# Kernel optimization log

Measured on AMD Instinct MI355X. Metric: run time of the kernel, lower is better.

The kernel has to match this reference:

```python
import jax, jax.numpy as jnp
import numpy as np

N_NODES = 100000
N_EDGES = 1600000
N_GRAPHS = 64
IN_DIM = 128
HIDDEN = 64
OUT_DIM = 6


def gcn_conv(x, W, b, src, dst, n_nodes):
    """PyG GCNConv: D^{-1/2} (A + I) D^{-1/2} X W + b (self-loops added)."""
    xw = x @ W  # [N, H]
    # degree including self-loop (computed over destination nodes)
    deg = jax.ops.segment_sum(jnp.ones((src.shape[0],), xw.dtype), dst,
                              num_segments=n_nodes) + 1.0
    dinv = jax.lax.rsqrt(deg)  # deg >= 1, always safe
    # per-edge normalized messages, scatter-add into destinations
    coef = (dinv[src] * dinv[dst])[:, None]  # [E, 1]
    agg = jax.ops.segment_sum(xw[src] * coef, dst, num_segments=n_nodes)
    # self-loop contribution: dinv[i]^2 * xw[i]
    agg = agg + xw * (dinv * dinv)[:, None]
    return agg + b


def setup_inputs() -> dict:
    key = jax.random.key(0)
    ks = jax.random.split(key, 9)
    x = jax.random.normal(ks[0], (N_NODES, IN_DIM), dtype=jnp.float32)
    edge_index = jax.random.randint(ks[1], (2, N_EDGES), 0, N_NODES, dtype=jnp.int64)
    batch = jnp.sort(jax.random.randint(ks[2], (N_NODES,), 0, N_GRAPHS, dtype=jnp.int64))
    # Glorot-ish params
    W1 = jax.random.normal(ks[3], (IN_DIM, HIDDEN), dtype=jnp.float32) / np.sqrt(IN_DIM)
    b1 = jnp.zeros((HIDDEN,), jnp.float32)
    W2 = jax.random.normal(ks[4], (HIDDEN, HIDDEN), dtype=jnp.float32) / np.sqrt(HIDDEN)
    b2 = jnp.zeros((HIDDEN,), jnp.float32)
    Wl = jax.random.normal(ks[5], (HIDDEN, OUT_DIM), dtype=jnp.float32) / np.sqrt(HIDDEN)
    bl = jnp.zeros((OUT_DIM,), jnp.float32)
    return {"x": x, "edge_index": edge_index, "batch": batch,
            "W1": W1, "b1": b1, "W2": W2, "b2": b2, "Wl": Wl, "bl": bl}


def reference(x, edge_index, batch, W1, b1, W2, b2, Wl, bl):
    src, dst = edge_index[0], edge_index[1]
    h = jax.nn.relu(gcn_conv(x, W1, b1, src, dst, N_NODES))
    # dropout is identity in eval mode
    h = gcn_conv(h, W2, b2, src, dst, N_NODES)
    # global mean pool over graph ids
    sums = jax.ops.segment_sum(h, batch, num_segments=N_GRAPHS)  # [G, H]
    cnts = jax.ops.segment_sum(jnp.ones((h.shape[0],), h.dtype), batch,
                               num_segments=N_GRAPHS)
    pooled = sums / jnp.maximum(cnts, 1.0)[:, None]
    return pooled @ Wl + bl  # [G, OUT_DIM]
```

## Files before the change

### kernel.cpp

```cpp
#include <hip/hip_runtime.h>

#define NCOL 64
#define BSH 8
#define NBMAX 512
#define EPB 2048
#define P2CAP 6144


__device__ __forceinline__ unsigned int bf16pair(float a, float b) {
  unsigned int ua = __float_as_uint(a), ub = __float_as_uint(b);
  ua = (ua + 0x7FFFu + ((ua >> 16) & 1u)) >> 16;
  ub = (ub + 0x7FFFu + ((ub >> 16) & 1u)) >> 16;
  return (ub << 16) | ua;
}
__device__ __forceinline__ float bf_lo(unsigned int v) { return __uint_as_float(v << 16); }
__device__ __forceinline__ float bf_hi(unsigned int v) { return __uint_as_float(v & 0xFFFF0000u); }


__global__ __launch_bounds__(256) void bin_p1(const int* __restrict__ src,
                                              const int* __restrict__ dst,
                                              unsigned int* __restrict__ ent,
                                              int* __restrict__ blockOff,
                                              int ne, int nb) {
  __shared__ int hist[NBMAX];
  __shared__ int base[NBMAX];
  __shared__ int part[256];
  __shared__ unsigned int stage[EPB];
  int tid = threadIdx.x;
  int e0 = blockIdx.x * EPB;
  int cnt = min(EPB, ne - e0);

  for (int i = tid; i < NBMAX; i += 256) hist[i] = 0;
  __syncthreads();
  for (int i = tid; i < cnt; i += 256) {
    int d = dst[e0 + i];
    atomicAdd(&hist[d >> BSH], 1);
  }
  __syncthreads();

  int a0 = hist[2 * tid], a1 = hist[2 * tid + 1];
  int s = a0 + a1;
  part[tid] = s;
  __syncthreads();
  for (int d = 1; d < 256; d <<= 1) {
    int v = (tid >= d) ? part[tid - d] : 0;
    __syncthreads();
    part[tid] += v;
    __syncthreads();
  }
  int off = part[tid] - s;
  base[2 * tid] = off;
  base[2 * tid + 1] = off + a0;
  __syncthreads();

  for (int b = tid; b < nb; b += 256) blockOff[(size_t)blockIdx.x * nb + b] = base[b];
  for (int i = tid; i < NBMAX; i += 256) hist[i] = base[i];
  __syncthreads();

  for (int i = tid; i < cnt; i += 256) {
    int d = dst[e0 + i];
    int sv = src[e0 + i];
    unsigned int e = ((unsigned int)(d & ((1 << BSH) - 1)) << 17) | (unsigned int)sv;
    int p = atomicAdd(&hist[d >> BSH], 1);
    stage[p] = e;
  }
  __syncthreads();
  for (int i = tid; i < cnt; i += 256) ent[e0 + i] = stage[i];
}


__global__ __launch_bounds__(256) void deg_bin(const unsigned int* __restrict__ ent,
                                               const int* __restrict__ blockOff,
                                               int* __restrict__ degi,
                                               int n, int ne, int nb, int nblk) {
  __shared__ int cnt[256];
  int b = blockIdx.x;
  int tid = threadIdx.x;
  cnt[tid] = 0;
  __syncthreads();
  for (int blk = tid; blk < nblk; blk += 256) {
    int e0 = blk * EPB;
    int bcnt = min(EPB, ne - e0);
    int st = blockOff[(size_t)blk * nb + b];
    int en = (b + 1 < nb) ? blockOff[(size_t)blk * nb + b + 1] : bcnt;
    for (int i = st; i < en; ++i) {
      unsigned int e = ent[e0 + i];
      atomicAdd(&cnt[e >> 17], 1);
    }
  }
  __syncthreads();
  int node = (b << BSH) + tid;
  if (node < n) degi[node] = cnt[tid];
}

__global__ void dinv_kernel(const int* __restrict__ degi, float* __restrict__ dinv, int n) {
  int i = blockIdx.x * blockDim.x + threadIdx.x;
  if (i < n) dinv[i] = rsqrtf((float)degi[i] + 1.0f);
}


__global__ void bounds_kernel(const int* __restrict__ batch, int* __restrict__ startg,
                              int* __restrict__ endg, int n) {
  int i = blockIdx.x * blockDim.x + threadIdx.x;
  if (i >= n) return;
  int b = batch[i];
  if (i == 0) {
    startg[b] = 0;
  } else {
    int bp = batch[i - 1];
    if (b != bp) { startg[b] = i; endg[bp] = i; }
  }
  if (i == n - 1) endg[b] = n;
}


#define SCAN_C 8

__global__ void scan_part(const int* __restrict__ degi, int* __restrict__ tsum,
                          int n, int nthreads) {
  int t = blockIdx.x * blockDim.x + threadIdx.x;
  if (t >= nthreads) return;
  int lo = t * SCAN_C, hi = min(lo + SCAN_C, n);
  int s = 0;
  for (int i = lo; i < hi; ++i) s += degi[i];
  tsum[t] = s;
}

__global__ void scan_mid(int* __restrict__ tsum, int* __restrict__ toff, int nthreads) {
  __shared__ int part[1024];
  int t = threadIdx.x;
  int chunk = (nthreads + 1023) >> 10;
  int lo = t * chunk, hi = min(lo + chunk, nthreads);
  int s = 0;
  for (int i = lo; i < hi; ++i) s += tsum[i];
  part[t] = s;
  __syncthreads();
  for (int d = 1; d < 1024; d <<= 1) {
    int v = (t >= d) ? part[t - d] : 0;
    __syncthreads();
    part[t] += v;
    __syncthreads();
  }
  int off = part[t] - s;
  for (int i = lo; i < hi; ++i) { toff[i] = off; off += tsum[i]; }
}

__global__ void scan_fill(const int* __restrict__ degi, const int* __restrict__ toff,
                          int* __restrict__ rowptr, int n, int nthreads) {
  int t = blockIdx.x * blockDim.x + threadIdx.x;
  if (t >= nthreads) return;
  int lo = t * SCAN_C, hi = min(lo + SCAN_C, n);
  int off = toff[t];
  for (int i = lo; i < hi; ++i) {
    rowptr[i] = off;
    off += degi[i];
  }
  if (hi == n) rowptr[n] = off;
}


__global__ __launch_bounds__(256) void bin_p2(const unsigned int* __restrict__ ent,
                                              const int* __restrict__ blockOff,
                                              const int* __restrict__ rowptr,
                                              int* __restrict__ csr_src,
                                              int n, int ne, int nb, int nblk) {
  __shared__ int cur[256];
  __shared__ int outS[P2CAP];
  int b = blockIdx.x;
  int tid = threadIdx.x;
  int node0 = b << BSH;
  int node1 = min(node0 + 256, n);
  int bucketBase = rowptr[node0];
  int bucketCnt = rowptr[node1] - bucketBase;
  int node = node0 + tid;
  cur[tid] = (node < node1) ? (rowptr[node] - bucketBase) : 0;
  __syncthreads();
  for (int blk = tid; blk < nblk; blk += 256) {
    int e0 = blk * EPB;
    int bcnt = min(EPB, ne - e0);
    int st = blockOff[(size_t)blk * nb + b];
    int en = (b + 1 < nb) ? blockOff[(size_t)blk * nb + b + 1] : bcnt;
    for (int i = st; i < en; ++i) {
      unsigned int e = ent[e0 + i];
      int dL = e >> 17;
      int sv = (int)(e & 0x1FFFFu);
      int p = atomicAdd(&cur[dL], 1);
      if (p < P2CAP) outS[p] = sv;
      else csr_src[bucketBase + p] = sv;
    }
  }
  __syncthreads();
  int lim = min(bucketCnt, P2CAP);
  for (int i = tid; i < lim; i += 256) csr_src[bucketBase + i] = outS[i];
}


template<int K>
__global__ __launch_bounds__(256, 4) void gemm_tiled(
    const float* __restrict__ X, const float* __restrict__ W,
    const float* __restrict__ dinv, unsigned int* __restrict__ Ybf, int n) {
  __shared__ float XS[64][65];
  __shared__ float WS[64][68];
  int tid = threadIdx.x;
  int rows0 = blockIdx.x * 64;
  int tr = tid & 15;
  int tc = tid >> 4;

  float acc[4][4];
#pragma unroll
  for (int i = 0; i < 4; ++i)
#pragma unroll
    for (int j = 0; j < 4; ++j) acc[i][j] = 0.f;

  int r0 = tid >> 4;
  int c4 = (tid & 15) * 4;

  for (int ks = 0; ks < K; ks += 64) {
    if (ks) __syncthreads();
#pragma unroll
    for (int it = 0; it < 4; ++it) {
      int r = r0 + it * 16;
      int gr2 = min(rows0 + r, n - 1);
      float4 v = *reinterpret_cast<const float4*>(X + (size_t)gr2 * K + ks + c4);
      XS[r][c4 + 0] = v.x; XS[r][c4 + 1] = v.y;
      XS[r][c4 + 2] = v.z; XS[r][c4 + 3] = v.w;
      float4 wv = *reinterpret_cast<const float4*>(W + (size_t)(ks + r) * NCOL + c4);
      WS[r][c4 + 0] = wv.x; WS[r][c4 + 1] = wv.y;
      WS[r][c4 + 2] = wv.z; WS[r][c4 + 3] = wv.w;
    }
    __syncthreads();

#pragma unroll 4
    for (int k = 0; k < 64; k += 2) {
      float a0 = XS[4 * tr + 0][k], a1 = XS[4 * tr + 1][k];
      float a2 = XS[4 * tr + 2][k], a3 = XS[4 * tr + 3][k];
      float b0 = XS[4 * tr + 0][k + 1], b1 = XS[4 * tr + 1][k + 1];
      float b2 = XS[4 * tr + 2][k + 1], b3 = XS[4 * tr + 3][k + 1];
      float4 w0 = *reinterpret_cast<const float4*>(&WS[k][4 * tc]);
      float4 w1 = *reinterpret_cast<const float4*>(&WS[k + 1][4 * tc]);
      acc[0][0] = fmaf(a0, w0.x, acc[0][0]); acc[0][1] = fmaf(a0, w0.y, acc[0][1]);
      acc[0][2] = fmaf(a0, w0.z, acc[0][2]); acc[0][3] = fmaf(a0, w0.w, acc[0][3]);
      acc[1][0] = fmaf(a1, w0.x, acc[1][0]); acc[1][1] = fmaf(a1, w0.y, acc[1][1]);
      acc[1][2] = fmaf(a1, w0.z, acc[1][2]); acc[1][3] = fmaf(a1, w0.w, acc[1][3]);
      acc[2][0] = fmaf(a2, w0.x, acc[2][0]); acc[2][1] = fmaf(a2, w0.y, acc[2][1]);
      acc[2][2] = fmaf(a2, w0.z, acc[2][2]); acc[2][3] = fmaf(a2, w0.w, acc[2][3]);
      acc[3][0] = fmaf(a3, w0.x, acc[3][0]); acc[3][1] = fmaf(a3, w0.y, acc[3][1]);
      acc[3][2] = fmaf(a3, w0.z, acc[3][2]); acc[3][3] = fmaf(a3, w0.w, acc[3][3]);
      acc[0][0] = fmaf(b0, w1.x, acc[0][0]); acc[0][1] = fmaf(b0, w1.y, acc[0][1]);
      acc[0][2] = fmaf(b0, w1.z, acc[0][2]); acc[0][3] = fmaf(b0, w1.w, acc[0][3]);
      acc[1][0] = fmaf(b1, w1.x, acc[1][0]); acc[1][1] = fmaf(b1, w1.y, acc[1][1]);
      acc[1][2] = fmaf(b1, w1.z, acc[1][2]); acc[1][3] = fmaf(b1, w1.w, acc[1][3]);
      acc[2][0] = fmaf(b2, w1.x, acc[2][0]); acc[2][1] = fmaf(b2, w1.y, acc[2][1]);
      acc[2][2] = fmaf(b2, w1.z, acc[2][2]); acc[2][3] = fmaf(b2, w1.w, acc[2][3]);
      acc[3][0] = fmaf(b3, w1.x, acc[3][0]); acc[3][1] = fmaf(b3, w1.y, acc[3][1]);
      acc[3][2] = fmaf(b3, w1.z, acc[3][2]); acc[3][3] = fmaf(b3, w1.w, acc[3][3]);
    }
  }

#pragma unroll
  for (int i = 0; i < 4; ++i) {
    int gr = rows0 + 4 * tr + i;
    if (gr < n) {
      float d = dinv[gr];
      uint2 o;
      o.x = bf16pair(acc[i][0] * d, acc[i][1] * d);
      o.y = bf16pair(acc[i][2] * d, acc[i][3] * d);
      *reinterpret_cast<uint2*>(Ybf + (size_t)gr * (NCOL / 2) + 2 * tc) = o;
    }
  }
}


template<bool RELU>
__global__ __launch_bounds__(256) void aggregate(
    const int* __restrict__ rowptr, const int* __restrict__ csr_src,
    const uint4* __restrict__ Ybf4, const float* __restrict__ dinv,
    const float* __restrict__ bias, float* __restrict__ H, int n) {
  int nd = (blockIdx.x * blockDim.x + threadIdx.x) >> 3;
  if (nd >= n) return;
  int l = threadIdx.x & 7;
  int lo = rowptr[nd], hi = rowptr[nd + 1];

  uint4 vs = Ybf4[(size_t)nd * 8 + l];
  float a0 = bf_lo(vs.x), a1 = bf_hi(vs.x);
  float a2 = bf_lo(vs.y), a3 = bf_hi(vs.y);
  float a4 = bf_lo(vs.z), a5 = bf_hi(vs.z);
  float a6 = bf_lo(vs.w), a7 = bf_hi(vs.w);

  int p = lo;
  for (; p + 3 < hi; p += 4) {
    int s0 = csr_src[p];
    int s1 = csr_src[p + 1];
    int s2 = csr_src[p + 2];
    int s3 = csr_src[p + 3];
    uint4 v0 = Ybf4[(size_t)s0 * 8 + l];
    uint4 v1 = Ybf4[(size_t)s1 * 8 + l];
    uint4 v2 = Ybf4[(size_t)s2 * 8 + l];
    uint4 v3 = Ybf4[(size_t)s3 * 8 + l];
    a0 += bf_lo(v0.x); a1 += bf_hi(v0.x);
    a2 += bf_lo(v0.y); a3 += bf_hi(v0.y);
    a4 += bf_lo(v0.z); a5 += bf_hi(v0.z);
    a6 += bf_lo(v0.w); a7 += bf_hi(v0.w);
    a0 += bf_lo(v1.x); a1 += bf_hi(v1.x);
    a2 += bf_lo(v1.y); a3 += bf_hi(v1.y);
    a4 += bf_lo(v1.z); a5 += bf_hi(v1.z);
    a6 += bf_lo(v1.w); a7 += bf_hi(v1.w);
    a0 += bf_lo(v2.x); a1 += bf_hi(v2.x);
    a2 += bf_lo(v2.y); a3 += bf_hi(v2.y);
    a4 += bf_lo(v2.z); a5 += bf_hi(v2.z);
    a6 += bf_lo(v2.w); a7 += bf_hi(v2.w);
    a0 += bf_lo(v3.x); a1 += bf_hi(v3.x);
    a2 += bf_lo(v3.y); a3 += bf_hi(v3.y);
    a4 += bf_lo(v3.z); a5 += bf_hi(v3.z);
    a6 += bf_lo(v3.w); a7 += bf_hi(v3.w);
  }
  for (; p < hi; ++p) {
    int s = csr_src[p];
    uint4 v = Ybf4[(size_t)s * 8 + l];
    a0 += bf_lo(v.x); a1 += bf_hi(v.x);
    a2 += bf_lo(v.y); a3 += bf_hi(v.y);
    a4 += bf_lo(v.z); a5 += bf_hi(v.z);
    a6 += bf_lo(v.w); a7 += bf_hi(v.w);
  }

  float d = dinv[nd];
  float4 b0 = *reinterpret_cast<const float4*>(bias + l * 8);
  float4 b1 = *reinterpret_cast<const float4*>(bias + l * 8 + 4);
  float4 o0, o1;
  o0.x = fmaf(d, a0, b0.x); o0.y = fmaf(d, a1, b0.y);
  o0.z = fmaf(d, a2, b0.z); o0.w = fmaf(d, a3, b0.w);
  o1.x = fmaf(d, a4, b1.x); o1.y = fmaf(d, a5, b1.y);
  o1.z = fmaf(d, a6, b1.z); o1.w = fmaf(d, a7, b1.w);
  if (RELU) {
    o0.x = fmaxf(o0.x, 0.f); o0.y = fmaxf(o0.y, 0.f);
    o0.z = fmaxf(o0.z, 0.f); o0.w = fmaxf(o0.w, 0.f);
    o1.x = fmaxf(o1.x, 0.f); o1.y = fmaxf(o1.y, 0.f);
    o1.z = fmaxf(o1.z, 0.f); o1.w = fmaxf(o1.w, 0.f);
  }
  float* hr = H + (size_t)nd * NCOL + l * 8;
  *reinterpret_cast<float4*>(hr) = o0;
  *reinterpret_cast<float4*>(hr + 4) = o1;
}


#define NPG 64

__global__ void pool_kernel(const float* __restrict__ H, const int* __restrict__ batch,
                            float* __restrict__ pool, int n) {
  int gid = (blockIdx.x * blockDim.x + threadIdx.x) >> 6;
  int c = threadIdx.x & 63;
  int n0 = gid * NPG;
  if (n0 >= n) return;
  int n1 = min(n0 + NPG, n);
  float acc = 0.f;
  int curg = batch[n0];
  for (int nd = n0; nd < n1; ++nd) {
    int g = batch[nd];
    if (g != curg) {
      atomicAdd(&pool[(size_t)curg * NCOL + c], acc);
      acc = 0.f;
      curg = g;
    }
    acc += H[(size_t)nd * NCOL + c];
  }
  atomicAdd(&pool[(size_t)curg * NCOL + c], acc);
}


__global__ void final_kernel(const float* __restrict__ pool, const int* __restrict__ startg,
                             const int* __restrict__ endg, const float* __restrict__ Wl,
                             const float* __restrict__ bl, float* __restrict__ out, int ng) {
  int t = threadIdx.x;
  if (t >= ng * 6) return;
  int g = t / 6, o = t % 6;
  float cntf = (float)(endg[g] - startg[g]);
  float inv = 1.0f / fmaxf(cntf, 1.0f);
  float s = 0.f;
#pragma unroll
  for (int c = 0; c < NCOL; ++c) s += pool[(size_t)g * NCOL + c] * Wl[c * 6 + o];
  out[t] = fmaf(s, inv, bl[o]);
}


extern "C" void kernel_launch(void* const* d_in, const int* in_sizes, int n_in,
                              void* d_out, int out_size, void* d_ws, size_t ws_size,
                              hipStream_t stream) {
  const float* x    = (const float*)d_in[0];
  const int*   ei   = (const int*)d_in[1];
  const int*   batch= (const int*)d_in[2];
  const float* W1   = (const float*)d_in[3];
  const float* b1   = (const float*)d_in[4];
  const float* W2   = (const float*)d_in[5];
  const float* b2   = (const float*)d_in[6];
  const float* Wl   = (const float*)d_in[7];
  const float* bl   = (const float*)d_in[8];
  float* out = (float*)d_out;

  int n  = in_sizes[0] / 128;
  int ne = in_sizes[1] / 2;
  int ng = out_size / 6;
  const int* srcI = ei;
  const int* dstI = ei + ne;

  int nb   = (n + 255) >> BSH;
  int nblk = (ne + EPB - 1) / EPB;

  char* w = (char*)d_ws;
  size_t o = 0;
  auto take = [&](size_t bytes) -> char* {
    char* p = w + o;
    o = (o + bytes + 255) & ~(size_t)255;
    return p;
  };
  float*        dinv    = (float*)take((size_t)n * 4);
  int*          degi    = (int*)  take((size_t)n * 4);
  int*          rowptr  = (int*)  take((size_t)(n + 1) * 4);
  int*          csr_src = (int*)  take((size_t)ne * 4);
  unsigned int* ent     = (unsigned int*)take((size_t)ne * 4);
  int*          blockOff= (int*)  take((size_t)nblk * nb * 4);
  unsigned int* Ybf     = (unsigned int*)take((size_t)n * (NCOL / 2) * 4);
  float*        H       = (float*)take((size_t)n * NCOL * 4);
  float*        pool    = (float*)take(4096 * 4);
  int*          startg  = (int*)  take(64 * 4);
  int*          endg    = (int*)  take(64 * 4);
  int*          tsum    = (int*)  take(16384 * 4);
  int*          toff    = (int*)  take(16384 * 4);

  hipMemsetAsync(pool, 0, 4096 * 4, stream);
  hipMemsetAsync(startg, 0, 64 * 4, stream);
  hipMemsetAsync(endg, 0, 64 * 4, stream);

  int nb256 = (n + 255) / 256;
  int nthreads = (n + SCAN_C - 1) / SCAN_C;
  int nbScan = (nthreads + 255) / 256;

  bin_p1<<<nblk, 256, 0, stream>>>(srcI, dstI, ent, blockOff, ne, nb);
  deg_bin<<<nb, 256, 0, stream>>>(ent, blockOff, degi, n, ne, nb, nblk);
  bounds_kernel<<<nb256, 256, 0, stream>>>(batch, startg, endg, n);
  dinv_kernel<<<nb256, 256, 0, stream>>>(degi, dinv, n);
  scan_part<<<nbScan, 256, 0, stream>>>(degi, tsum, n, nthreads);
  scan_mid<<<1, 1024, 0, stream>>>(tsum, toff, nthreads);
  scan_fill<<<nbScan, 256, 0, stream>>>(degi, toff, rowptr, n, nthreads);
  bin_p2<<<nb, 256, 0, stream>>>(ent, blockOff, rowptr, csr_src, n, ne, nb, nblk);

  int nbAgg = (n * 8 + 255) / 256;
  int nbGemm = (n + 63) / 64;

  gemm_tiled<128><<<nbGemm, 256, 0, stream>>>(x, W1, dinv, Ybf, n);
  aggregate<true><<<nbAgg, 256, 0, stream>>>(rowptr, csr_src, (const uint4*)Ybf, dinv, b1, H, n);

  gemm_tiled<64><<<nbGemm, 256, 0, stream>>>(H, W2, dinv, Ybf, n);
  aggregate<false><<<nbAgg, 256, 0, stream>>>(rowptr, csr_src, (const uint4*)Ybf, dinv, b2, H, n);

  int ngroups = (n + NPG - 1) / NPG;
  int pblocks = (ngroups * 64 + 255) / 256;
  pool_kernel<<<pblocks, 256, 0, stream>>>(H, batch, pool, n);
  final_kernel<<<1, 384, 0, stream>>>(pool, startg, endg, Wl, bl, out, ng);
}
```

Measured before the change: 240.5 us.

## Replace FP32 tiled GEMM with bf16 MFMA GEMM for node feature transforms

The shared-memory FP32 FMA GEMM is replaced by a kernel that converts X and W to bf16 in registers and uses the 16x16x32 bf16 MFMA instruction. Each wave computes a 16-column slice over 64 rows, then results are scaled by dinv, staged through LDS and written out as coalesced 16-byte stores. This removes the FP32 ALU and LDS traffic of the old kernel. In exchange, inputs are rounded to bf16 before the multiply, which lowers accuracy, and each block reads W directly from global memory with strided loads.

```diff
diff --git a/kernel.cpp b/kernel.cpp
--- a/kernel.cpp
+++ b/kernel.cpp
@@ -6,6 +6,9 @@
 #define EPB 2048
 #define P2CAP 6144
 
+typedef __attribute__((ext_vector_type(8))) short bf16x8;
+typedef __attribute__((ext_vector_type(4))) float f32x4;
+
 
 __device__ __forceinline__ unsigned int bf16pair(float a, float b) {
   unsigned int ua = __float_as_uint(a), ub = __float_as_uint(b);
@@ -15,6 +18,11 @@
 }
 __device__ __forceinline__ float bf_lo(unsigned int v) { return __uint_as_float(v << 16); }
 __device__ __forceinline__ float bf_hi(unsigned int v) { return __uint_as_float(v & 0xFFFF0000u); }
+__device__ __forceinline__ unsigned short bfs(float x) {
+  unsigned int u = __float_as_uint(x);
+  u = (u + 0x7FFFu + ((u >> 16) & 1u)) >> 16;
+  return (unsigned short)u;
+}
 
 
 __global__ __launch_bounds__(256) void bin_p1(const int* __restrict__ src,
@@ -196,77 +204,65 @@
 
 
 template<int K>
-__global__ __launch_bounds__(256, 4) void gemm_tiled(
+__global__ __launch_bounds__(256, 8) void gemm_mfma(
     const float* __restrict__ X, const float* __restrict__ W,
     const float* __restrict__ dinv, unsigned int* __restrict__ Ybf, int n) {
-  __shared__ float XS[64][65];
-  __shared__ float WS[64][68];
+  __shared__ unsigned short YS[64][64];
   int tid = threadIdx.x;
+  int w = tid >> 6;
+  int l = tid & 63;
+  int lr = l & 15;
+  int lk = l >> 4;
   int rows0 = blockIdx.x * 64;
-  int tr = tid & 15;
-  int tc = tid >> 4;
-
-  float acc[4][4];
-#pragma unroll
-  for (int i = 0; i < 4; ++i)
-#pragma unroll
-    for (int j = 0; j < 4; ++j) acc[i][j] = 0.f;
-
-  int r0 = tid >> 4;
-  int c4 = (tid & 15) * 4;
-
-  for (int ks = 0; ks < K; ks += 64) {
-    if (ks) __syncthreads();
-#pragma unroll
-    for (int it = 0; it < 4; ++it) {
-      int r = r0 + it * 16;
-      int gr2 = min(rows0 + r, n - 1);
-      float4 v = *reinterpret_cast<const float4*>(X + (size_t)gr2 * K + ks + c4);
-      XS[r][c4 + 0] = v.x; XS[r][c4 + 1] = v.y;
-      XS[r][c4 + 2] = v.z; XS[r][c4 + 3] = v.w;
-      float4 wv = *reinterpret_cast<const float4*>(W + (size_t)(ks + r) * NCOL + c4);
-      WS[r][c4 + 0] = wv.x; WS[r][c4 + 1] = wv.y;
-      WS[r][c4 + 2] = wv.z; WS[r][c4 + 3] = wv.w;
-    }
-    __syncthreads();
-
-#pragma unroll 4
-    for (int k = 0; k < 64; k += 2) {
-      float a0 = XS[4 * tr + 0][k], a1 = XS[4 * tr + 1][k];
-      float a2 = XS[4 * tr + 2][k], a3 = XS[4 * tr + 3][k];
-      float b0 = XS[4 * tr + 0][k + 1], b1 = XS[4 * tr + 1][k + 1];
-      float b2 = XS[4 * tr + 2][k + 1], b3 = XS[4 * tr + 3][k + 1];
-      float4 w0 = *reinterpret_cast<const float4*>(&WS[k][4 * tc]);
-      float4 w1 = *reinterpret_cast<const float4*>(&WS[k + 1][4 * tc]);
-      acc[0][0] = fmaf(a0, w0.x, acc[0][0]); acc[0][1] = fmaf(a0, w0.y, acc[0][1]);
-      acc[0][2] = fmaf(a0, w0.z, acc[0][2]); acc[0][3] = fmaf(a0, w0.w, acc[0][3]);
-      acc[1][0] = fmaf(a1, w0.x, acc[1][0]); acc[1][1] = fmaf(a1, w0.y, acc[1][1]);
-      acc[1][2] = fmaf(a1, w0.z, acc[1][2]); acc[1][3] = fmaf(a1, w0.w, acc[1][3]);
-      acc[2][0] = fmaf(a2, w0.x, acc[2][0]); acc[2][1] = fmaf(a2, w0.y, acc[2][1]);
-      acc[2][2] = fmaf(a2, w0.z, acc[2][2]); acc[2][3] = fmaf(a2, w0.w, acc[2][3]);
-      acc[3][0] = fmaf(a3, w0.x, acc[3][0]); acc[3][1] = fmaf(a3, w0.y, acc[3][1]);
-      acc[3][2] = fmaf(a3, w0.z, acc[3][2]); acc[3][3] = fmaf(a3, w0.w, acc[3][3]);
-      acc[0][0] = fmaf(b0, w1.x, acc[0][0]); acc[0][1] = fmaf(b0, w1.y, acc[0][1]);
-      acc[0][2] = fmaf(b0, w1.z, acc[0][2]); acc[0][3] = fmaf(b0, w1.w, acc[0][3]);
-      acc[1][0] = fmaf(b1, w1.x, acc[1][0]); acc[1][1] = fmaf(b1, w1.y, acc[1][1]);
-      acc[1][2] = fmaf(b1, w1.z, acc[1][2]); acc[1][3] = fmaf(b1, w1.w, acc[1][3]);
-      acc[2][0] = fmaf(b2, w1.x, acc[2][0]); acc[2][1] = fmaf(b2, w1.y, acc[2][1]);
-      acc[2][2] = fmaf(b2, w1.z, acc[2][2]); acc[2][3] = fmaf(b2, w1.w, acc[2][3]);
-      acc[3][0] = fmaf(b3, w1.x, acc[3][0]); acc[3][1] = fmaf(b3, w1.y, acc[3][1]);
-      acc[3][2] = fmaf(b3, w1.z, acc[3][2]); acc[3][3] = fmaf(b3, w1.w, acc[3][3]);
-    }
-  }
-
-#pragma unroll
-  for (int i = 0; i < 4; ++i) {
-    int gr = rows0 + 4 * tr + i;
-    if (gr < n) {
-      float d = dinv[gr];
-      uint2 o;
-      o.x = bf16pair(acc[i][0] * d, acc[i][1] * d);
-      o.y = bf16pair(acc[i][2] * d, acc[i][3] * d);
-      *reinterpret_cast<uint2*>(Ybf + (size_t)gr * (NCOL / 2) + 2 * tc) = o;
-    }
+
+  bf16x8 bfrag[K / 32];
+#pragma unroll
+  for (int s = 0; s < K / 32; ++s) {
+#pragma unroll
+    for (int j = 0; j < 8; ++j) {
+      int k = s * 32 + lk * 8 + j;
+      bfrag[s][j] = (short)bfs(W[(size_t)k * NCOL + 16 * w + lr]);
+    }
+  }
+
+  f32x4 acc[4];
+#pragma unroll
+  for (int rt = 0; rt < 4; ++rt) acc[rt] = (f32x4){0.f, 0.f, 0.f, 0.f};
+
+#pragma unroll
+  for (int rt = 0; rt < 4; ++rt) {
+    int row = min(rows0 + rt * 16 + lr, n - 1);
+    const float* xr = X + (size_t)row * K + lk * 8;
+#pragma unroll
+    for (int s = 0; s < K / 32; ++s) {
+      float4 x0 = *reinterpret_cast<const float4*>(xr + s * 32);
+      float4 x1 = *reinterpret_cast<const float4*>(xr + s * 32 + 4);
+      bf16x8 af;
+      af[0] = (short)bfs(x0.x); af[1] = (short)bfs(x0.y);
+      af[2] = (short)bfs(x0.z); af[3] = (short)bfs(x0.w);
+      af[4] = (short)bfs(x1.x); af[5] = (short)bfs(x1.y);
+      af[6] = (short)bfs(x1.z); af[7] = (short)bfs(x1.w);
+      acc[rt] = __builtin_amdgcn_mfma_f32_16x16x32_bf16(af, bfrag[s], acc[rt], 0, 0, 0);
+    }
+  }
+
+#pragma unroll
+  for (int rt = 0; rt < 4; ++rt) {
+#pragma unroll
+    for (int j = 0; j < 4; ++j) {
+      int row = rt * 16 + lk * 4 + j;
+      float d = dinv[min(rows0 + row, n - 1)];
+      YS[row][16 * w + lr] = bfs(acc[rt][j] * d);
+    }
+  }
+  __syncthreads();
+
+  const uint4* ys4 = reinterpret_cast<const uint4*>(&YS[0][0]);
+  for (int idx = tid; idx < 512; idx += 256) {
+    int row = idx >> 3;
+    int gr = rows0 + row;
+    if (gr < n)
+      reinterpret_cast<uint4*>(Ybf + (size_t)gr * 32)[idx & 7] = ys4[idx];
   }
 }
 
@@ -446,10 +442,10 @@
   int nbAgg = (n * 8 + 255) / 256;
   int nbGemm = (n + 63) / 64;
 
-  gemm_tiled<128><<<nbGemm, 256, 0, stream>>>(x, W1, dinv, Ybf, n);
+  gemm_mfma<128><<<nbGemm, 256, 0, stream>>>(x, W1, dinv, Ybf, n);
   aggregate<true><<<nbAgg, 256, 0, stream>>>(rowptr, csr_src, (const uint4*)Ybf, dinv, b1, H, n);
 
-  gemm_tiled<64><<<nbGemm, 256, 0, stream>>>(H, W2, dinv, Ybf, n);
+  gemm_mfma<64><<<nbGemm, 256, 0, stream>>>(H, W2, dinv, Ybf, n);
   aggregate<false><<<nbAgg, 256, 0, stream>>>(rowptr, csr_src, (const uint4*)Ybf, dinv, b2, H, n);
 
   int ngroups = (n + NPG - 1) / NPG;
```

After: 231.3 us. 1.04x faster.
